# Kernel tuning notes

Hardware: AMD Instinct MI355X
Metric: run time of the kernel (lower is better)

## Reference

```python
import jax, jax.numpy as jnp
import numpy as np

B, N, D, C = 2, 65536, 128, 128          # batch, n_entries, input_dim, channel_dim
DEG, N_ACTIVE, STRIDE = 16, 4096, 16     # ring-neighbor sparse structure


def _build_indices():
    """Replicates the original module's Python intersection loops exactly,
    flattening them into (src_i, src_j, pair_out) gather/scatter index arrays.
    k[:, e, :] = sum_m a[:, i_th[m], :] * b[:, j_th[m], :] for each write slot e.
    Each slot e is written exactly once, so scatter-add == the original set."""
    neigh = [[] for _ in range(N)]
    for t in range(N_ACTIVE):
        i = t * STRIDE
        neigh[i] = [((t + dlt) % N_ACTIVE) * STRIDE for dlt in range(1, DEG + 1)]
    src_i, src_j, out = [], [], []
    e = 0
    for i in range(N):
        if not neigh[i]:
            continue
        i_element = list(neigh[i]) + [i]
        i_set = set(i_element)
        for j in neigh[i]:
            j_list = neigh[j]
            j_set = set(j_list)
            j_th = [m for m in j_list if m in i_set]      # order of j's list
            i_th = [m for m in i_element if m in j_set]   # order of i_element
            for ai, bi in zip(i_th, j_th):
                src_i.append(ai)
                src_j.append(bi)
                out.append(e)
            e += 1
    return (np.asarray(src_i, np.int32), np.asarray(src_j, np.int32),
            np.asarray(out, np.int32))


def setup_inputs() -> dict:
    key = jax.random.key(0)
    ks = jax.random.split(key, 8)
    s = 1.0 / np.sqrt(D)
    src_i, src_j, pair_out = _build_indices()
    return {
        "x": jax.random.normal(ks[0], (B, N, D), jnp.float32),
        "ln_in_w": jnp.ones((D,), jnp.float32),
        "ln_in_b": jnp.zeros((D,), jnp.float32),
        "Wla": jax.random.normal(ks[1], (C, D), jnp.float32) * s,
        "bla": jnp.zeros((C,), jnp.float32),
        "Wga": jax.random.normal(ks[2], (C, D), jnp.float32) * s,
        "bga": jnp.zeros((C,), jnp.float32),
        "Wlb": jax.random.normal(ks[3], (C, D), jnp.float32) * s,
        "blb": jnp.zeros((C,), jnp.float32),
        "Wgb": jax.random.normal(ks[4], (C, D), jnp.float32) * s,
        "bgb": jnp.zeros((C,), jnp.float32),
        "ln_o_w": jnp.ones((C,), jnp.float32),
        "ln_o_b": jnp.zeros((C,), jnp.float32),
        "Wgo": jax.random.normal(ks[5], (D, D), jnp.float32) * s,
        "bgo": jnp.zeros((D,), jnp.float32),
        "Wlo": jax.random.normal(ks[6], (D, C), jnp.float32) * s,
        "blo": jnp.zeros((D,), jnp.float32),
        "src_i": jnp.asarray(src_i),
        "src_j": jnp.asarray(src_j),
        "pair_out": jnp.asarray(pair_out),
    }


def _layernorm(x, w, b, eps=1e-5):
    mu = jnp.mean(x, axis=-1, keepdims=True)
    var = jnp.mean(jnp.square(x - mu), axis=-1, keepdims=True)
    return (x - mu) * jax.lax.rsqrt(var + eps) * w + b


def reference(x, ln_in_w, ln_in_b, Wla, bla, Wga, bga, Wlb, blb, Wgb, bgb,
              ln_o_w, ln_o_b, Wgo, bgo, Wlo, blo, src_i, src_j, pair_out):
    xn = _layernorm(x, ln_in_w, ln_in_b)                              # [B,N,D]
    a = jax.nn.sigmoid(xn @ Wga.T + bga) * (xn @ Wla.T + bla)         # [B,N,C]
    b = jax.nn.sigmoid(xn @ Wgb.T + bgb) * (xn @ Wlb.T + blb)         # [B,N,C]
    # triangular update: gather-multiply-sum-scatter over precomputed pairs
    prod = a[:, src_i, :] * b[:, src_j, :]                            # [B,P,C]
    k = jnp.zeros_like(a).at[:, pair_out, :].add(prod)                # [B,N,C]
    out = jax.nn.sigmoid(xn @ Wgo.T + bgo) * (_layernorm(k, ln_o_w, ln_o_b) @ Wlo.T + blo)
    return out
```

## Files before the change

kernel.cpp:

```cpp
#include <hip/hip_runtime.h>


#define BB 2
#define NN 65536
#define DD 128
#define CC 128
#define NA 4096
#define STR 16
#define WSZ 16384

typedef short short4v __attribute__((ext_vector_type(4)));
typedef short short8v __attribute__((ext_vector_type(8)));
typedef __bf16 bf16x8 __attribute__((ext_vector_type(8)));
typedef float f32x4 __attribute__((ext_vector_type(4)));

__device__ __forceinline__ float sigf(float v) { return 1.0f / (1.0f + __expf(-v)); }
__device__ __forceinline__ short nbf(float f) {
    union { __bf16 h; short s; } u; u.h = (__bf16)f; return u.s;
}
__device__ __forceinline__ float bf2f(short b) {
    union { unsigned u; float f; } v; v.u = ((unsigned)(unsigned short)b) << 16;
    return v.f;
}
__device__ __forceinline__ bf16x8 s2b(short8v s) {
    union { short8v s; bf16x8 b; } u; u.s = s; return u.b;
}

__global__ __launch_bounds__(256)
void kern_wcvt(const float* __restrict__ Wla, const float* __restrict__ Wga,
               const float* __restrict__ Wlb, const float* __restrict__ Wgb,
               const float* __restrict__ Wgo, const float* __restrict__ Wlo,
               const float* __restrict__ lnw, const float* __restrict__ lnb,
               const float* __restrict__ lnow, const float* __restrict__ lnob,
               const float* __restrict__ bla, const float* __restrict__ bga,
               const float* __restrict__ blb, const float* __restrict__ bgb,
               const float* __restrict__ bgo, const float* __restrict__ blo,
               short* __restrict__ wbf, float* __restrict__ vtab)
{
    const int b = blockIdx.x;
    if (b < 64) {
        const int i  = b * 256 + threadIdx.x;
        const int ch = i >> 7, d = i & 127;
        const int pos = ((ch >> 4) * 4 + (d >> 5)) * 512
                      + ((((d >> 3) & 3) * 16 + (ch & 15)) * 8) + (d & 7);
        const float wi = lnw[d], wo = lnow[d];
        wbf[pos]           = nbf(Wla[i] * wi);
        wbf[WSZ + pos]     = nbf(Wga[i] * wi);
        wbf[2 * WSZ + pos] = nbf(Wlb[i] * wi);
        wbf[3 * WSZ + pos] = nbf(Wgb[i] * wi);
        wbf[4 * WSZ + pos] = nbf(Wgo[i] * wi);
        wbf[5 * WSZ + pos] = nbf(Wlo[i] * wo);
    } else {
        const int t = (b - 64) * 256 + threadIdx.x;
        const int m = t >> 7, c = t & 127;
        const float* Wr = (m == 0) ? Wla : (m == 1) ? Wga : (m == 2) ? Wlb
                        : (m == 3) ? Wgb : (m == 4) ? Wgo : Wlo;
        const float* bb = (m == 5) ? lnob : lnb;
        const float* bi = (m == 0) ? bla : (m == 1) ? bga : (m == 2) ? blb
                        : (m == 3) ? bgb : (m == 4) ? bgo : blo;
        const float* row = Wr + (size_t)c * DD;
        float acc = 0.f;
        for (int d = 0; d < DD; d += 4) {
            const f32x4 w4 = *(const f32x4*)(row + d);
            const f32x4 b4 = *(const f32x4*)(bb + d);
            acc += w4[0]*b4[0] + w4[1]*b4[1] + w4[2]*b4[2] + w4[3]*b4[3];
        }
        vtab[m * 128 + c] = acc + bi[c];
    }
}

__global__ __launch_bounds__(64)
void kern_ab(const float* __restrict__ x, const short* __restrict__ wbf,
             const float* __restrict__ vtab, float* __restrict__ cbuf)
{
    const int l     = threadIdx.x;
    const int bid   = blockIdx.x;
    const int batch = bid >> 9;
    const int t0    = ((bid & 511) >> 1) << 4;
    const int nt0   = (bid & 1) * 4;
    const int lr    = l & 15;
    const int q     = l >> 4;
    const int fl    = l * 8;

    const float* xr = x + ((size_t)batch * NN + (size_t)(t0 + lr) * STR) * DD + q * 8;
    f32x4 v[4][2];
    #pragma unroll
    for (int kk = 0; kk < 4; ++kk) {
        v[kk][0] = *(const f32x4*)(xr + kk * 32);
        v[kk][1] = *(const f32x4*)(xr + kk * 32 + 4);
    }
    float s = 0.f, ss = 0.f;
    #pragma unroll
    for (int kk = 0; kk < 4; ++kk)
        #pragma unroll
        for (int h = 0; h < 2; ++h)
            #pragma unroll
            for (int j = 0; j < 4; ++j) { const float f = v[kk][h][j]; s += f; ss += f * f; }
    s += __shfl_xor(s, 16); ss += __shfl_xor(ss, 16);
    s += __shfl_xor(s, 32); ss += __shfl_xor(ss, 32);
    const float mu = s * (1.0f / 128.0f);
    const float rs = rsqrtf(ss * (1.0f / 128.0f) - mu * mu + 1e-5f);
    const float p  = -mu * rs;

    bf16x8 af[4];
    #pragma unroll
    for (int kk = 0; kk < 4; ++kk) {
        short8v t;
        #pragma unroll
        for (int j = 0; j < 4; ++j) {
            t[j]     = nbf(v[kk][0][j] * rs + p);
            t[4 + j] = nbf(v[kk][1][j] * rs + p);
        }
        af[kk] = s2b(t);
    }

    const short* wla = wbf;
    const short* wga = wbf + WSZ;
    const short* wlb = wbf + 2 * WSZ;
    const short* wgb = wbf + 3 * WSZ;

    #pragma unroll
    for (int nt = 0; nt < 4; ++nt) {
        const int col  = (nt0 + nt) * 16 + lr;
        const int base = ((nt0 + nt) * 4) * 512 + fl;
        f32x4 ala = {0.f,0.f,0.f,0.f}, aga = {0.f,0.f,0.f,0.f};
        f32x4 alb = {0.f,0.f,0.f,0.f}, agb = {0.f,0.f,0.f,0.f};
        #pragma unroll
        for (int kk = 0; kk < 4; ++kk) {
            const int o = base + kk * 512;
            ala = __builtin_amdgcn_mfma_f32_16x16x32_bf16(af[kk], *(const bf16x8*)(wla + o), ala, 0, 0, 0);
            aga = __builtin_amdgcn_mfma_f32_16x16x32_bf16(af[kk], *(const bf16x8*)(wga + o), aga, 0, 0, 0);
            alb = __builtin_amdgcn_mfma_f32_16x16x32_bf16(af[kk], *(const bf16x8*)(wlb + o), alb, 0, 0, 0);
            agb = __builtin_amdgcn_mfma_f32_16x16x32_bf16(af[kk], *(const bf16x8*)(wgb + o), agb, 0, 0, 0);
        }
        const float vla = vtab[col], vga = vtab[128 + col];
        const float vlb = vtab[256 + col], vgb = vtab[384 + col];
        #pragma unroll
        for (int r = 0; r < 4; ++r) {
            const float av = sigf(aga[r] + vga) * (ala[r] + vla);
            const float bv = sigf(agb[r] + vgb) * (alb[r] + vlb);
            cbuf[((size_t)batch * NA + t0 + q * 4 + r) * CC + col] = av * bv;
        }
    }
}

__global__ __launch_bounds__(64)
void kern_out(const float* __restrict__ x, const short* __restrict__ wbf,
              const float* __restrict__ vtab, const float* __restrict__ cbuf,
              float* __restrict__ out)
{
    __shared__ short kls[2][16][136];
    const int bid   = blockIdx.x;
    const int swz   = (bid & 7) * 512 + (bid >> 3);
    const int batch = swz >> 11;
    const int ib    = swz & 2047;
    const int row0  = ib * 32;
    const int t0    = ib * 2;

    const int l  = threadIdx.x;
    const int lr = l & 15, lk = l >> 4;
    const int fl = l * 8;

    bf16x8 afx[2][4];
    #pragma unroll
    for (int g = 0; g < 2; ++g) {
        const float* xr = x + ((size_t)batch * NN + row0 + g * 16 + lr) * DD + lk * 8;
        f32x4 v[4][2];
        #pragma unroll
        for (int kk = 0; kk < 4; ++kk) {
            v[kk][0] = *(const f32x4*)(xr + kk * 32);
            v[kk][1] = *(const f32x4*)(xr + kk * 32 + 4);
        }
        float s = 0.f, ss = 0.f;
        #pragma unroll
        for (int kk = 0; kk < 4; ++kk)
            #pragma unroll
            for (int h = 0; h < 2; ++h)
                #pragma unroll
                for (int j = 0; j < 4; ++j) { const float f = v[kk][h][j]; s += f; ss += f * f; }
        s += __shfl_xor(s, 16); ss += __shfl_xor(ss, 16);
        s += __shfl_xor(s, 32); ss += __shfl_xor(ss, 32);
        const float mu = s * (1.0f / 128.0f);
        const float rs = rsqrtf(ss * (1.0f / 128.0f) - mu * mu + 1e-5f);
        const float p  = -mu * rs;
        #pragma unroll
        for (int kk = 0; kk < 4; ++kk) {
            short8v o;
            #pragma unroll
            for (int j = 0; j < 4; ++j) {
                o[j]     = nbf(v[kk][0][j] * rs + p);
                o[4 + j] = nbf(v[kk][1][j] * rs + p);
            }
            afx[g][kk] = s2b(o);
        }
    }

    {
        const int sg = l >> 5;
        const int c4 = (l & 31) * 4;
        const int t  = t0 + sg;
        f32x4 cv[15];
        #pragma unroll
        for (int sx = 0; sx < 15; ++sx)
            cv[sx] = *(const f32x4*)(cbuf + ((size_t)batch * NA + ((t + sx + 2) & (NA - 1))) * CC + c4);
        short4v z = {0, 0, 0, 0};
        *(short4v*)&kls[sg][15][c4] = z;
        float s0 = 0.f, s1 = 0.f, s2 = 0.f, s3 = 0.f;
        #pragma unroll
        for (int sx = 14; sx >= 0; --sx) {
            s0 += cv[sx][0]; s1 += cv[sx][1]; s2 += cv[sx][2]; s3 += cv[sx][3];
            short4v o; o[0] = nbf(s0); o[1] = nbf(s1); o[2] = nbf(s2); o[3] = nbf(s3);
            *(short4v*)&kls[sg][sx][c4] = o;
        }
    }

    bf16x8 afk[2][4];
    #pragma unroll
    for (int g = 0; g < 2; ++g) {
        short8v kraw[4];
        #pragma unroll
        for (int kk = 0; kk < 4; ++kk)
            kraw[kk] = *(const short8v*)&kls[g][lr][kk * 32 + lk * 8];
        float ks = 0.f, kss = 0.f;
        #pragma unroll
        for (int kk = 0; kk < 4; ++kk)
            #pragma unroll
            for (int j = 0; j < 8; ++j) { const float f = bf2f(kraw[kk][j]); ks += f; kss += f * f; }
        ks += __shfl_xor(ks, 16); kss += __shfl_xor(kss, 16);
        ks += __shfl_xor(ks, 32); kss += __shfl_xor(kss, 32);
        const float kmu = ks * (1.0f / 128.0f);
        const float krs = rsqrtf(kss * (1.0f / 128.0f) - kmu * kmu + 1e-5f);
        const float kp  = -kmu * krs;
        #pragma unroll
        for (int kk = 0; kk < 4; ++kk) {
            short8v o;
            #pragma unroll
            for (int j = 0; j < 8; ++j)
                o[j] = nbf(bf2f(kraw[kk][j]) * krs + kp);
            afk[g][kk] = s2b(o);
        }
    }

    const short* wgo = wbf + 4 * WSZ;
    const short* wlo = wbf + 5 * WSZ;
    const float* vgo = vtab + 4 * 128;
    const float* vlo = vtab + 5 * 128;
    #pragma unroll
    for (int nt = 0; nt < 8; ++nt) {
        bf16x8 bg_[4], bh_[4];
        #pragma unroll
        for (int kk = 0; kk < 4; ++kk) {
            bg_[kk] = *(const bf16x8*)(wgo + (nt * 4 + kk) * 512 + fl);
            bh_[kk] = *(const bf16x8*)(wlo + (nt * 4 + kk) * 512 + fl);
        }
        f32x4 ag0 = {0.f,0.f,0.f,0.f}, ag1 = {0.f,0.f,0.f,0.f};
        f32x4 ah0 = {0.f,0.f,0.f,0.f}, ah1 = {0.f,0.f,0.f,0.f};
        #pragma unroll
        for (int kk = 0; kk < 4; ++kk) {
            ag0 = __builtin_amdgcn_mfma_f32_16x16x32_bf16(afx[0][kk], bg_[kk], ag0, 0, 0, 0);
            ag1 = __builtin_amdgcn_mfma_f32_16x16x32_bf16(afx[1][kk], bg_[kk], ag1, 0, 0, 0);
            ah0 = __builtin_amdgcn_mfma_f32_16x16x32_bf16(afk[0][kk], bh_[kk], ah0, 0, 0, 0);
            ah1 = __builtin_amdgcn_mfma_f32_16x16x32_bf16(afk[1][kk], bh_[kk], ah1, 0, 0, 0);
        }
        const int   col = nt * 16 + lr;
        const float vg  = vgo[col];
        const float vl  = vlo[col];
        #pragma unroll
        for (int r = 0; r < 4; ++r) {
            const size_t rowa = (size_t)batch * NN + row0 + lk * 4 + r;
            out[rowa * DD + col]        = sigf(ag0[r] + vg) * (ah0[r] + vl);
            out[(rowa + 16) * DD + col] = sigf(ag1[r] + vg) * (ah1[r] + vl);
        }
    }
}

extern "C" void kernel_launch(void* const* d_in, const int* in_sizes, int n_in,
                              void* d_out, int out_size, void* d_ws, size_t ws_size,
                              hipStream_t stream)
{
    const float* x    = (const float*)d_in[0];
    const float* lnw  = (const float*)d_in[1];
    const float* lnb  = (const float*)d_in[2];
    const float* Wla  = (const float*)d_in[3];
    const float* bla  = (const float*)d_in[4];
    const float* Wga  = (const float*)d_in[5];
    const float* bga  = (const float*)d_in[6];
    const float* Wlb  = (const float*)d_in[7];
    const float* blb  = (const float*)d_in[8];
    const float* Wgb  = (const float*)d_in[9];
    const float* bgb  = (const float*)d_in[10];
    const float* lnow = (const float*)d_in[11];
    const float* lnob = (const float*)d_in[12];
    const float* Wgo  = (const float*)d_in[13];
    const float* bgo  = (const float*)d_in[14];
    const float* Wlo  = (const float*)d_in[15];
    const float* blo  = (const float*)d_in[16];

    float* cbuf = (float*)d_ws;
    short* wbf  = (short*)((char*)d_ws + (size_t)BB * NA * CC * 4);
    float* vtab = (float*)((char*)wbf + 6 * WSZ * sizeof(short));
    float* out  = (float*)d_out;

    hipLaunchKernelGGL(kern_wcvt, dim3(67), dim3(256), 0, stream,
                       Wla, Wga, Wlb, Wgb, Wgo, Wlo,
                       lnw, lnb, lnow, lnob,
                       bla, bga, blb, bgb, bgo, blo, wbf, vtab);
    hipLaunchKernelGGL(kern_ab, dim3(BB * 512), dim3(64), 0, stream,
                       x, wbf, vtab, cbuf);
    hipLaunchKernelGGL(kern_out, dim3(BB * 2048), dim3(64), 0, stream,
                       x, wbf, vtab, cbuf, out);
}
```

Baseline: 51.72 us.

## Halve kern_out tile to 16 rows per block and keep suffix sums in fp32 LDS

kern_out now handles one active index t (16 rows) per 64-thread block rather than two, which doubles the grid to 8192 blocks and shrinks per-thread register state. The suffix-sum k rows are now kept in fp32 in LDS instead of bf16, removing a bf16 round-trip before the output layernorm. The prefetch of the cbuf window is also issued alongside the x loads. In exchange, the Wgo/Wlo weight fragments are reloaded for every 16 rows instead of being shared across 32, and each block now does the full 15-row cbuf window reduction for a single t.

```diff
diff --git a/kernel.cpp b/kernel.cpp
--- a/kernel.cpp
+++ b/kernel.cpp
@@ -9,18 +9,14 @@
 #define STR 16
 #define WSZ 16384
 
-typedef short short4v __attribute__((ext_vector_type(4)));
 typedef short short8v __attribute__((ext_vector_type(8)));
 typedef __bf16 bf16x8 __attribute__((ext_vector_type(8)));
 typedef float f32x4 __attribute__((ext_vector_type(4)));
+typedef float f32x2 __attribute__((ext_vector_type(2)));
 
 __device__ __forceinline__ float sigf(float v) { return 1.0f / (1.0f + __expf(-v)); }
 __device__ __forceinline__ short nbf(float f) {
     union { __bf16 h; short s; } u; u.h = (__bf16)f; return u.s;
-}
-__device__ __forceinline__ float bf2f(short b) {
-    union { unsigned u; float f; } v; v.u = ((unsigned)(unsigned short)b) << 16;
-    return v.f;
 }
 __device__ __forceinline__ bf16x8 s2b(short8v s) {
     union { short8v s; bf16x8 b; } u; u.s = s; return u.b;
@@ -149,28 +145,45 @@
               const float* __restrict__ vtab, const float* __restrict__ cbuf,
               float* __restrict__ out)
 {
-    __shared__ short kls[2][16][136];
+    __shared__ float kls[16][132];
     const int bid   = blockIdx.x;
-    const int swz   = (bid & 7) * 512 + (bid >> 3);
-    const int batch = swz >> 11;
-    const int ib    = swz & 2047;
-    const int row0  = ib * 32;
-    const int t0    = ib * 2;
+    const int swz   = (bid & 7) * 1024 + (bid >> 3);
+    const int batch = swz >> 12;
+    const int t     = swz & 4095;
+    const int row0  = t * 16;
 
     const int l  = threadIdx.x;
     const int lr = l & 15, lk = l >> 4;
     const int fl = l * 8;
 
-    bf16x8 afx[2][4];
-    #pragma unroll
-    for (int g = 0; g < 2; ++g) {
-        const float* xr = x + ((size_t)batch * NN + row0 + g * 16 + lr) * DD + lk * 8;
-        f32x4 v[4][2];
-        #pragma unroll
-        for (int kk = 0; kk < 4; ++kk) {
-            v[kk][0] = *(const f32x4*)(xr + kk * 32);
-            v[kk][1] = *(const f32x4*)(xr + kk * 32 + 4);
-        }
+    const float* xr = x + ((size_t)batch * NN + row0 + lr) * DD + lk * 8;
+    f32x4 v[4][2];
+    #pragma unroll
+    for (int kk = 0; kk < 4; ++kk) {
+        v[kk][0] = *(const f32x4*)(xr + kk * 32);
+        v[kk][1] = *(const f32x4*)(xr + kk * 32 + 4);
+    }
+
+    const int c2 = l * 2;
+    f32x2 cv[15];
+    #pragma unroll
+    for (int sx = 14; sx >= 0; --sx)
+        cv[sx] = *(const f32x2*)(cbuf + ((size_t)batch * NA + ((t + sx + 2) & (NA - 1))) * CC + c2);
+
+    {
+        f32x2 z = {0.f, 0.f};
+        *(f32x2*)&kls[15][c2] = z;
+        float s0 = 0.f, s1 = 0.f;
+        #pragma unroll
+        for (int sx = 14; sx >= 0; --sx) {
+            s0 += cv[sx][0]; s1 += cv[sx][1];
+            f32x2 o = {s0, s1};
+            *(f32x2*)&kls[sx][c2] = o;
+        }
+    }
+
+    bf16x8 afx[4];
+    {
         float s = 0.f, ss = 0.f;
         #pragma unroll
         for (int kk = 0; kk < 4; ++kk)
@@ -191,41 +204,25 @@
                 o[j]     = nbf(v[kk][0][j] * rs + p);
                 o[4 + j] = nbf(v[kk][1][j] * rs + p);
             }
-            afx[g][kk] = s2b(o);
-        }
-    }
-
+            afx[kk] = s2b(o);
+        }
+    }
+
+    bf16x8 afk[4];
     {
-        const int sg = l >> 5;
-        const int c4 = (l & 31) * 4;
-        const int t  = t0 + sg;
-        f32x4 cv[15];
-        #pragma unroll
-        for (int sx = 0; sx < 15; ++sx)
-            cv[sx] = *(const f32x4*)(cbuf + ((size_t)batch * NA + ((t + sx + 2) & (NA - 1))) * CC + c4);
-        short4v z = {0, 0, 0, 0};
-        *(short4v*)&kls[sg][15][c4] = z;
-        float s0 = 0.f, s1 = 0.f, s2 = 0.f, s3 = 0.f;
-        #pragma unroll
-        for (int sx = 14; sx >= 0; --sx) {
-            s0 += cv[sx][0]; s1 += cv[sx][1]; s2 += cv[sx][2]; s3 += cv[sx][3];
-            short4v o; o[0] = nbf(s0); o[1] = nbf(s1); o[2] = nbf(s2); o[3] = nbf(s3);
-            *(short4v*)&kls[sg][sx][c4] = o;
-        }
-    }
-
-    bf16x8 afk[2][4];
-    #pragma unroll
-    for (int g = 0; g < 2; ++g) {
-        short8v kraw[4];
+        f32x4 kr[4][2];
+        #pragma unroll
+        for (int kk = 0; kk < 4; ++kk) {
+            kr[kk][0] = *(const f32x4*)&kls[lr][kk * 32 + lk * 8];
+            kr[kk][1] = *(const f32x4*)&kls[lr][kk * 32 + lk * 8 + 4];
+        }
+        float ks = 0.f, kss = 0.f;
         #pragma unroll
         for (int kk = 0; kk < 4; ++kk)
-            kraw[kk] = *(const short8v*)&kls[g][lr][kk * 32 + lk * 8];
-        float ks = 0.f, kss = 0.f;
-        #pragma unroll
-        for (int kk = 0; kk < 4; ++kk)
-            #pragma unroll
-            for (int j = 0; j < 8; ++j) { const float f = bf2f(kraw[kk][j]); ks += f; kss += f * f; }
+            #pragma unroll
+            for (int h = 0; h < 2; ++h)
+                #pragma unroll
+                for (int j = 0; j < 4; ++j) { const float f = kr[kk][h][j]; ks += f; kss += f * f; }
         ks += __shfl_xor(ks, 16); kss += __shfl_xor(kss, 16);
         ks += __shfl_xor(ks, 32); kss += __shfl_xor(kss, 32);
         const float kmu = ks * (1.0f / 128.0f);
@@ -235,9 +232,11 @@
         for (int kk = 0; kk < 4; ++kk) {
             short8v o;
             #pragma unroll
-            for (int j = 0; j < 8; ++j)
-                o[j] = nbf(bf2f(kraw[kk][j]) * krs + kp);
-            afk[g][kk] = s2b(o);
+            for (int j = 0; j < 4; ++j) {
+                o[j]     = nbf(kr[kk][0][j] * krs + kp);
+                o[4 + j] = nbf(kr[kk][1][j] * krs + kp);
+            }
+            afk[kk] = s2b(o);
         }
     }
 
@@ -247,20 +246,12 @@
     const float* vlo = vtab + 5 * 128;
     #pragma unroll
     for (int nt = 0; nt < 8; ++nt) {
-        bf16x8 bg_[4], bh_[4];
-        #pragma unroll
-        for (int kk = 0; kk < 4; ++kk) {
-            bg_[kk] = *(const bf16x8*)(wgo + (nt * 4 + kk) * 512 + fl);
-            bh_[kk] = *(const bf16x8*)(wlo + (nt * 4 + kk) * 512 + fl);
-        }
-        f32x4 ag0 = {0.f,0.f,0.f,0.f}, ag1 = {0.f,0.f,0.f,0.f};
-        f32x4 ah0 = {0.f,0.f,0.f,0.f}, ah1 = {0.f,0.f,0.f,0.f};
-        #pragma unroll
-        for (int kk = 0; kk < 4; ++kk) {
-            ag0 = __builtin_amdgcn_mfma_f32_16x16x32_bf16(afx[0][kk], bg_[kk], ag0, 0, 0, 0);
-            ag1 = __builtin_amdgcn_mfma_f32_16x16x32_bf16(afx[1][kk], bg_[kk], ag1, 0, 0, 0);
-            ah0 = __builtin_amdgcn_mfma_f32_16x16x32_bf16(afk[0][kk], bh_[kk], ah0, 0, 0, 0);
-            ah1 = __builtin_amdgcn_mfma_f32_16x16x32_bf16(afk[1][kk], bh_[kk], ah1, 0, 0, 0);
+        f32x4 ag = {0.f,0.f,0.f,0.f}, ah = {0.f,0.f,0.f,0.f};
+        #pragma unroll
+        for (int kk = 0; kk < 4; ++kk) {
+            const int o = (nt * 4 + kk) * 512 + fl;
+            ag = __builtin_amdgcn_mfma_f32_16x16x32_bf16(afx[kk], *(const bf16x8*)(wgo + o), ag, 0, 0, 0);
+            ah = __builtin_amdgcn_mfma_f32_16x16x32_bf16(afk[kk], *(const bf16x8*)(wlo + o), ah, 0, 0, 0);
         }
         const int   col = nt * 16 + lr;
         const float vg  = vgo[col];
@@ -268,8 +259,7 @@
         #pragma unroll
         for (int r = 0; r < 4; ++r) {
             const size_t rowa = (size_t)batch * NN + row0 + lk * 4 + r;
-            out[rowa * DD + col]        = sigf(ag0[r] + vg) * (ah0[r] + vl);
-            out[(rowa + 16) * DD + col] = sigf(ag1[r] + vg) * (ah1[r] + vl);
+            out[rowa * DD + col] = sigf(ag[r] + vg) * (ah[r] + vl);
         }
     }
 }
@@ -307,6 +297,6 @@
                        bla, bga, blb, bgb, bgo, blo, wbf, vtab);
     hipLaunchKernelGGL(kern_ab, dim3(BB * 512), dim3(64), 0, stream,
                        x, wbf, vtab, cbuf);
-    hipLaunchKernelGGL(kern_out, dim3(BB * 2048), dim3(64), 0, stream,
+    hipLaunchKernelGGL(kern_out, dim3(BB * 4096), dim3(64), 0, stream,
                        x, wbf, vtab, cbuf, out);
 }
```

Result: no change. 52.21 us (+0.9%).

## Fold output layernorm scaling into the GEMM epilogue and regroup kernel_ab into 4-wave blocks

Applied to the files above, without the earlier changes.

kern_out now feeds the raw bf16 prefix sums of k straight into the MFMA. It applies the layernorm scale and shift per row in the epilogue through a precomputed column sum of the weights, which stores a second vtab table. The cbuf loads are moved up to overlap with the x loads, and kern_ab packs four wavefronts per 256-thread block. This removes a per-element normalize-and-convert pass, at the cost of feeding unnormalized values into bf16 and some extra LDS traffic for the row statistics.

```diff
diff --git a/kernel.cpp b/kernel.cpp
--- a/kernel.cpp
+++ b/kernel.cpp
@@ -13,6 +13,7 @@
 typedef short short8v __attribute__((ext_vector_type(8)));
 typedef __bf16 bf16x8 __attribute__((ext_vector_type(8)));
 typedef float f32x4 __attribute__((ext_vector_type(4)));
+typedef float f32x2 __attribute__((ext_vector_type(2)));
 
 __device__ __forceinline__ float sigf(float v) { return 1.0f / (1.0f + __expf(-v)); }
 __device__ __forceinline__ short nbf(float f) {
@@ -56,25 +57,30 @@
         const float* Wr = (m == 0) ? Wla : (m == 1) ? Wga : (m == 2) ? Wlb
                         : (m == 3) ? Wgb : (m == 4) ? Wgo : Wlo;
         const float* bb = (m == 5) ? lnob : lnb;
+        const float* ww = (m == 5) ? lnow : lnw;
         const float* bi = (m == 0) ? bla : (m == 1) ? bga : (m == 2) ? blb
                         : (m == 3) ? bgb : (m == 4) ? bgo : blo;
         const float* row = Wr + (size_t)c * DD;
-        float acc = 0.f;
+        float av = 0.f, as = 0.f;
         for (int d = 0; d < DD; d += 4) {
             const f32x4 w4 = *(const f32x4*)(row + d);
             const f32x4 b4 = *(const f32x4*)(bb + d);
-            acc += w4[0]*b4[0] + w4[1]*b4[1] + w4[2]*b4[2] + w4[3]*b4[3];
-        }
-        vtab[m * 128 + c] = acc + bi[c];
-    }
-}
-
-__global__ __launch_bounds__(64)
+            const f32x4 g4 = *(const f32x4*)(ww + d);
+            av += w4[0]*b4[0] + w4[1]*b4[1] + w4[2]*b4[2] + w4[3]*b4[3];
+            as += w4[0]*g4[0] + w4[1]*g4[1] + w4[2]*g4[2] + w4[3]*g4[3];
+        }
+        vtab[m * 128 + c]       = av + bi[c];
+        vtab[768 + m * 128 + c] = as;
+    }
+}
+
+__global__ __launch_bounds__(256)
 void kern_ab(const float* __restrict__ x, const short* __restrict__ wbf,
              const float* __restrict__ vtab, float* __restrict__ cbuf)
 {
-    const int l     = threadIdx.x;
-    const int bid   = blockIdx.x;
+    const int wv    = threadIdx.x >> 6;
+    const int l     = threadIdx.x & 63;
+    const int bid   = blockIdx.x * 4 + wv;
     const int batch = bid >> 9;
     const int t0    = ((bid & 511) >> 1) << 4;
     const int nt0   = (bid & 1) * 4;
@@ -150,6 +156,7 @@
               float* __restrict__ out)
 {
     __shared__ short kls[2][16][136];
+    __shared__ float kst[2][16][2];
     const int bid   = blockIdx.x;
     const int swz   = (bid & 7) * 512 + (bid >> 3);
     const int batch = swz >> 11;
@@ -161,23 +168,47 @@
     const int lr = l & 15, lk = l >> 4;
     const int fl = l * 8;
 
-    bf16x8 afx[2][4];
+    f32x4 v[2][4][2];
     #pragma unroll
     for (int g = 0; g < 2; ++g) {
         const float* xr = x + ((size_t)batch * NN + row0 + g * 16 + lr) * DD + lk * 8;
-        f32x4 v[4][2];
-        #pragma unroll
-        for (int kk = 0; kk < 4; ++kk) {
-            v[kk][0] = *(const f32x4*)(xr + kk * 32);
-            v[kk][1] = *(const f32x4*)(xr + kk * 32 + 4);
-        }
+        #pragma unroll
+        for (int kk = 0; kk < 4; ++kk) {
+            v[g][kk][0] = *(const f32x4*)(xr + kk * 32);
+            v[g][kk][1] = *(const f32x4*)(xr + kk * 32 + 4);
+        }
+    }
+
+    const int sg = l >> 5;
+    const int c4 = (l & 31) * 4;
+    const int t  = t0 + sg;
+    f32x4 cv[15];
+    #pragma unroll
+    for (int sx = 14; sx >= 0; --sx)
+        cv[sx] = *(const f32x4*)(cbuf + ((size_t)batch * NA + ((t + sx + 2) & (NA - 1))) * CC + c4);
+
+    {
+        short4v z = {0, 0, 0, 0};
+        *(short4v*)&kls[sg][15][c4] = z;
+        float s0 = 0.f, s1 = 0.f, s2 = 0.f, s3 = 0.f;
+        #pragma unroll
+        for (int sx = 14; sx >= 0; --sx) {
+            s0 += cv[sx][0]; s1 += cv[sx][1]; s2 += cv[sx][2]; s3 += cv[sx][3];
+            short4v o; o[0] = nbf(s0); o[1] = nbf(s1); o[2] = nbf(s2); o[3] = nbf(s3);
+            *(short4v*)&kls[sg][sx][c4] = o;
+        }
+    }
+
+    bf16x8 afx[2][4];
+    #pragma unroll
+    for (int g = 0; g < 2; ++g) {
         float s = 0.f, ss = 0.f;
         #pragma unroll
         for (int kk = 0; kk < 4; ++kk)
             #pragma unroll
             for (int h = 0; h < 2; ++h)
                 #pragma unroll
-                for (int j = 0; j < 4; ++j) { const float f = v[kk][h][j]; s += f; ss += f * f; }
+                for (int j = 0; j < 4; ++j) { const float f = v[g][kk][h][j]; s += f; ss += f * f; }
         s += __shfl_xor(s, 16); ss += __shfl_xor(ss, 16);
         s += __shfl_xor(s, 32); ss += __shfl_xor(ss, 32);
         const float mu = s * (1.0f / 128.0f);
@@ -188,63 +219,48 @@
             short8v o;
             #pragma unroll
             for (int j = 0; j < 4; ++j) {
-                o[j]     = nbf(v[kk][0][j] * rs + p);
-                o[4 + j] = nbf(v[kk][1][j] * rs + p);
+                o[j]     = nbf(v[g][kk][0][j] * rs + p);
+                o[4 + j] = nbf(v[g][kk][1][j] * rs + p);
             }
             afx[g][kk] = s2b(o);
         }
     }
 
-    {
-        const int sg = l >> 5;
-        const int c4 = (l & 31) * 4;
-        const int t  = t0 + sg;
-        f32x4 cv[15];
-        #pragma unroll
-        for (int sx = 0; sx < 15; ++sx)
-            cv[sx] = *(const f32x4*)(cbuf + ((size_t)batch * NA + ((t + sx + 2) & (NA - 1))) * CC + c4);
-        short4v z = {0, 0, 0, 0};
-        *(short4v*)&kls[sg][15][c4] = z;
-        float s0 = 0.f, s1 = 0.f, s2 = 0.f, s3 = 0.f;
-        #pragma unroll
-        for (int sx = 14; sx >= 0; --sx) {
-            s0 += cv[sx][0]; s1 += cv[sx][1]; s2 += cv[sx][2]; s3 += cv[sx][3];
-            short4v o; o[0] = nbf(s0); o[1] = nbf(s1); o[2] = nbf(s2); o[3] = nbf(s3);
-            *(short4v*)&kls[sg][sx][c4] = o;
-        }
-    }
-
     bf16x8 afk[2][4];
+    short8v kraw[2][4];
+    #pragma unroll
+    for (int g = 0; g < 2; ++g)
+        #pragma unroll
+        for (int kk = 0; kk < 4; ++kk) {
+            kraw[g][kk] = *(const short8v*)&kls[g][lr][kk * 32 + lk * 8];
+            afk[g][kk]  = s2b(kraw[g][kk]);
+        }
+
     #pragma unroll
     for (int g = 0; g < 2; ++g) {
-        short8v kraw[4];
-        #pragma unroll
-        for (int kk = 0; kk < 4; ++kk)
-            kraw[kk] = *(const short8v*)&kls[g][lr][kk * 32 + lk * 8];
         float ks = 0.f, kss = 0.f;
         #pragma unroll
         for (int kk = 0; kk < 4; ++kk)
             #pragma unroll
-            for (int j = 0; j < 8; ++j) { const float f = bf2f(kraw[kk][j]); ks += f; kss += f * f; }
+            for (int j = 0; j < 8; ++j) { const float f = bf2f(kraw[g][kk][j]); ks += f; kss += f * f; }
         ks += __shfl_xor(ks, 16); kss += __shfl_xor(kss, 16);
         ks += __shfl_xor(ks, 32); kss += __shfl_xor(kss, 32);
         const float kmu = ks * (1.0f / 128.0f);
         const float krs = rsqrtf(kss * (1.0f / 128.0f) - kmu * kmu + 1e-5f);
-        const float kp  = -kmu * krs;
-        #pragma unroll
-        for (int kk = 0; kk < 4; ++kk) {
-            short8v o;
-            #pragma unroll
-            for (int j = 0; j < 8; ++j)
-                o[j] = nbf(bf2f(kraw[kk][j]) * krs + kp);
-            afk[g][kk] = s2b(o);
-        }
-    }
+        if (lk == 0) { kst[g][lr][0] = krs; kst[g][lr][1] = -kmu * krs; }
+    }
+    f32x2 kp[2][4];
+    #pragma unroll
+    for (int g = 0; g < 2; ++g)
+        #pragma unroll
+        for (int r = 0; r < 4; ++r)
+            kp[g][r] = *(const f32x2*)&kst[g][lk * 4 + r][0];
 
     const short* wgo = wbf + 4 * WSZ;
     const short* wlo = wbf + 5 * WSZ;
     const float* vgo = vtab + 4 * 128;
     const float* vlo = vtab + 5 * 128;
+    const float* slo = vtab + 768 + 5 * 128;
     #pragma unroll
     for (int nt = 0; nt < 8; ++nt) {
         bf16x8 bg_[4], bh_[4];
@@ -265,11 +281,14 @@
         const int   col = nt * 16 + lr;
         const float vg  = vgo[col];
         const float vl  = vlo[col];
+        const float sl  = slo[col];
         #pragma unroll
         for (int r = 0; r < 4; ++r) {
             const size_t rowa = (size_t)batch * NN + row0 + lk * 4 + r;
-            out[rowa * DD + col]        = sigf(ag0[r] + vg) * (ah0[r] + vl);
-            out[(rowa + 16) * DD + col] = sigf(ag1[r] + vg) * (ah1[r] + vl);
+            const float h0 = kp[0][r][0] * ah0[r] + (kp[0][r][1] * sl + vl);
+            const float h1 = kp[1][r][0] * ah1[r] + (kp[1][r][1] * sl + vl);
+            out[rowa * DD + col]        = sigf(ag0[r] + vg) * h0;
+            out[(rowa + 16) * DD + col] = sigf(ag1[r] + vg) * h1;
         }
     }
 }
@@ -305,7 +324,7 @@
                        Wla, Wga, Wlb, Wgb, Wgo, Wlo,
                        lnw, lnb, lnow, lnob,
                        bla, bga, blb, bgb, bgo, blo, wbf, vtab);
-    hipLaunchKernelGGL(kern_ab, dim3(BB * 512), dim3(64), 0, stream,
+    hipLaunchKernelGGL(kern_ab, dim3(BB * 128), dim3(256), 0, stream,
                        x, wbf, vtab, cbuf);
     hipLaunchKernelGGL(kern_out, dim3(BB * 2048), dim3(64), 0, stream,
                        x, wbf, vtab, cbuf, out);
```

After: 56.67 us. +9.6%, slower.
